# Optimization experiments

Hardware: AMD Instinct MI355X
Metric: run time of the kernel (lower is better)

Reference implementation:

```python
import jax, jax.numpy as jnp
import numpy as np

N = 100_000   # nodes
E = 640_000   # edges
H = 128       # hidden_dim
L = 4         # num_layers
C = 2         # num_classes
G = 128       # graphs in batch

def setup_inputs() -> dict:
    key = jax.random.key(0)
    ks = jax.random.split(key, 8)
    x = jax.random.randint(ks[0], (N, 1), 0, 2)
    edge_index = jax.random.randint(ks[1], (2, E), 0, N)
    batch = jnp.sort(jax.random.randint(ks[2], (N,), 0, G))
    embed = jax.random.normal(ks[3], (2, H), jnp.float32)
    Ws = jax.random.normal(ks[4], (L, H, H), jnp.float32) * (1.0 / np.sqrt(H))
    bs = jnp.zeros((L, H), jnp.float32)
    W_out = jax.random.normal(ks[5], (H, C), jnp.float32) * (1.0 / np.sqrt(H))
    b_out = jnp.zeros((C,), jnp.float32)
    return dict(x=x, edge_index=edge_index, batch=batch, embed=embed,
                Ws=Ws, bs=bs, W_out=W_out, b_out=b_out)

def reference(x, edge_index, batch, embed, Ws, bs, W_out, b_out):
    src, dst = edge_index[0], edge_index[1]
    # symmetric GCN normalization with self-loops (PyG GCNConv default)
    deg = jax.ops.segment_sum(jnp.ones(E, jnp.float32), dst, num_segments=N) + 1.0
    dinv = jax.lax.rsqrt(deg)
    enorm = (dinv[src] * dinv[dst])[:, None]   # per-edge norm
    snorm = (dinv * dinv)[:, None]             # self-loop norm

    h = embed[x[:, 0]]                          # [N, H] embedding lookup
    n_layers = Ws.shape[0]
    for l in range(n_layers):
        t = h @ Ws[l]                           # linear transform [N, H]
        agg = jax.ops.segment_sum(t[src] * enorm, dst, num_segments=N) \
              + t * snorm + bs[l]
        h = jax.nn.relu(agg) if l < n_layers - 1 else agg

    # global mean pool over graph ids
    counts = jax.ops.segment_sum(jnp.ones(N, jnp.float32), batch, num_segments=G)
    pooled = jax.ops.segment_sum(h, batch, num_segments=G) \
             / jnp.maximum(counts, 1.0)[:, None]   # [G, H]
    return pooled @ W_out + b_out                  # [G, C]
```

## Files before the change

kernel.cpp:

```cpp
#include <hip/hip_runtime.h>

typedef __attribute__((ext_vector_type(8))) short bf16x8;
typedef __attribute__((ext_vector_type(4))) float f32x4;
typedef __attribute__((ext_vector_type(2))) float f32x2;

__device__ inline unsigned short bf16_rtn(float f) {
  unsigned u = __float_as_uint(f);
  unsigned r = u + 0x7fffu + ((u >> 16) & 1u);
  return (unsigned short)(r >> 16);
}

__device__ inline void split_bf16(float f, unsigned short& hi, unsigned short& lo) {
  hi = bf16_rtn(f);
  float fh = __uint_as_float((unsigned)hi << 16);
  lo = bf16_rtn(f - fh);
}

__device__ inline float bf16_to_f(unsigned short v) {
  return __uint_as_float((unsigned)v << 16);
}

__device__ inline unsigned char f_to_fp8(float f) {
  int r = __builtin_amdgcn_cvt_pk_fp8_f32(f, f, 0, false);
  return (unsigned char)(r & 0xff);
}
__device__ inline f32x2 fp8x2_to_f(unsigned short v) {
  return __builtin_amdgcn_cvt_pk_f32_fp8((int)v, false);
}

__global__ void k_init(int* __restrict__ deg, int* __restrict__ gpz, int N, int M,
                       const float* __restrict__ Ws, const float* __restrict__ embed,
                       unsigned short* __restrict__ wphi,
                       unsigned short* __restrict__ wplo,
                       float* __restrict__ T) {
  int i = blockIdx.x * 256 + threadIdx.x;
  if (i < N) deg[i] = 0;
  if (i < M) gpz[i] = 0;
  int l = blockIdx.x;
  if (l < 3) {
    const float* W = Ws + (size_t)(l + 1) * 128 * 128;
    unsigned short* dh = wphi + (size_t)l * 16384;
    unsigned short* dl = wplo + (size_t)l * 16384;
    for (int idx = threadIdx.x; idx < 16384; idx += 256) {
      int j = idx & 7;
      int lane = (idx >> 3) & 63;
      int c = (idx >> 9) & 3;
      int ct = idx >> 11;
      int k = c * 32 + ((lane >> 4) * 8) + j;
      int n = ct * 16 + (lane & 15);
      unsigned short hi, lo;
      split_bf16(W[k * 128 + n], hi, lo);
      dh[idx] = hi;
      dl[idx] = lo;
    }
  } else if (l == 3) {
    int t = threadIdx.x;
    int r = t >> 7, c = t & 127;
    float acc = 0.f;
    for (int k = 0; k < 128; ++k)
      acc += embed[r * 128 + k] * Ws[k * 128 + c];
    T[r * 128 + c] = acc;
  }
}


__global__ void k_hist(const int* __restrict__ dst, int* __restrict__ deg,
                       int* __restrict__ posr, int E) {
  int e = blockIdx.x * 256 + threadIdx.x;
  if (e < E) posr[e] = atomicAdd(&deg[dst[e]], 1);
}

__global__ void k_scan1(const int* __restrict__ deg, int* __restrict__ rowptr,
                        int* __restrict__ bsum, float* __restrict__ dpk,
                        const int* __restrict__ x, const int* __restrict__ batch,
                        int* __restrict__ gstart, int* __restrict__ gend, int N) {
  __shared__ int s[256];
  int t = threadIdx.x;
  int i = blockIdx.x * 256 + t;
  int v = (i < N) ? deg[i] : 0;
  if (i < N) {
    float di = rsqrtf((float)v + 1.0f);
    dpk[i] = x[i] ? -di : di;
    int g = batch[i];
    if (i == 0 || batch[i - 1] != g) gstart[g] = i;
    if (i == N - 1 || batch[i + 1] != g) gend[g] = i + 1;
  }
  s[t] = v;
  __syncthreads();
  for (int off = 1; off < 256; off <<= 1) {
    int u = (t >= off) ? s[t - off] : 0;
    __syncthreads();
    s[t] += u;
    __syncthreads();
  }
  if (i < N) rowptr[i] = s[t] - v;
  if (t == 255) bsum[blockIdx.x] = s[255];
}

__global__ void k_scan2(const int* __restrict__ bsum, int* __restrict__ boff, int nb) {
  __shared__ int s[512];
  int t = threadIdx.x;
  int v = (t < nb) ? bsum[t] : 0;
  s[t] = v;
  __syncthreads();
  for (int off = 1; off < 512; off <<= 1) {
    int u = (t >= off) ? s[t - off] : 0;
    __syncthreads();
    s[t] += u;
    __syncthreads();
  }
  boff[t] = s[t] - v;
}

__global__ void k_scan3(int* __restrict__ rowptr, const int* __restrict__ boff,
                        int N, int E) {
  int i = blockIdx.x * 256 + threadIdx.x;
  if (i < N) rowptr[i] += boff[i >> 8];
  if (i == 0) rowptr[N] = E;
}

__global__ void k_scatter(const int* __restrict__ src, const int* __restrict__ dst,
                          const int* __restrict__ posr, const int* __restrict__ rowptr,
                          const float* __restrict__ dpk,
                          int2* __restrict__ epack, int E) {
  int e = blockIdx.x * 256 + threadIdx.x;
  if (e >= E) return;
  int s = src[e], d = dst[e];
  int pos = rowptr[d] + posr[e];
  epack[pos] = make_int2(s, __float_as_int(dpk[s]));
}

__device__ inline void gather_node(const unsigned char* __restrict__ tin,
                                   const int2* __restrict__ epack,
                                   int r0, int deg, int lane,
                                   float& a0, float& a1) {
  int dcap = deg < 64 ? deg : 64;
  int sl = 0;
  if (lane < dcap) sl = epack[r0 + lane].x;
  a0 = 0.f; a1 = 0.f;
  int e = 0;
  for (; e + 4 <= dcap; e += 4) {
    int s0 = __shfl(sl, e, 64),     s1 = __shfl(sl, e + 1, 64);
    int s2 = __shfl(sl, e + 2, 64), s3 = __shfl(sl, e + 3, 64);
    unsigned short p0 = *(const unsigned short*)(tin + (size_t)s0 * 128 + 2 * lane);
    unsigned short p1 = *(const unsigned short*)(tin + (size_t)s1 * 128 + 2 * lane);
    unsigned short p2 = *(const unsigned short*)(tin + (size_t)s2 * 128 + 2 * lane);
    unsigned short p3 = *(const unsigned short*)(tin + (size_t)s3 * 128 + 2 * lane);
    f32x2 v0 = fp8x2_to_f(p0), v1 = fp8x2_to_f(p1);
    f32x2 v2 = fp8x2_to_f(p2), v3 = fp8x2_to_f(p3);
    a0 += v0.x + v1.x + v2.x + v3.x;
    a1 += v0.y + v1.y + v2.y + v3.y;
  }
  for (; e < dcap; ++e) {
    int s = __shfl(sl, e, 64);
    unsigned short p = *(const unsigned short*)(tin + (size_t)s * 128 + 2 * lane);
    f32x2 v = fp8x2_to_f(p);
    a0 += v.x;
    a1 += v.y;
  }
  for (int ee = r0 + 64; ee < r0 + deg; ++ee) {
    int s = epack[ee].x;
    unsigned short p = *(const unsigned short*)(tin + (size_t)s * 128 + 2 * lane);
    f32x2 v = fp8x2_to_f(p);
    a0 += v.x;
    a1 += v.y;
  }
}

__global__ void k_agg(const unsigned char* __restrict__ tin,
                      const int* __restrict__ rowptr,
                      const int2* __restrict__ epack,
                      const float* __restrict__ dpk, const float* __restrict__ bvec,
                      unsigned short* __restrict__ h, int N) {
  int i = (blockIdx.x * blockDim.x + threadIdx.x) >> 6;
  int lane = threadIdx.x & 63;
  if (i >= N) return;
  int r0 = rowptr[i], r1 = rowptr[i + 1];
  unsigned short ps = *(const unsigned short*)(tin + (size_t)i * 128 + 2 * lane);
  float dp = dpk[i];
  float2 bv = *(const float2*)(bvec + 2 * lane);
  float a0, a1;
  gather_node(tin, epack, r0, r1 - r0, lane, a0, a1);
  f32x2 sv = fp8x2_to_f(ps);
  float di = fabsf(dp);
  a0 = fmaxf(di * (a0 + sv.x) + bv.x, 0.f);
  a1 = fmaxf(di * (a1 + sv.y) + bv.y, 0.f);
  *(unsigned*)(h + (size_t)i * 128 + 2 * lane) =
      (unsigned)bf16_rtn(a0) | ((unsigned)bf16_rtn(a1) << 16);
}

__global__ void k_agg_pool(const unsigned char* __restrict__ tin,
                           const int* __restrict__ rowptr,
                           const int2* __restrict__ epack,
                           const float* __restrict__ dpk, const float* __restrict__ bvec,
                           const int* __restrict__ batch,
                           float* __restrict__ pooled, int N) {
  __shared__ float sh[4][128];
  __shared__ int sg[4];
  int wave = threadIdx.x >> 6;
  int lane = threadIdx.x & 63;
  int i = blockIdx.x * 4 + wave;
  if (threadIdx.x < 4) sg[threadIdx.x] = -1;
  __syncthreads();
  if (i < N) {
    int r0 = rowptr[i], r1 = rowptr[i + 1];
    unsigned short ps = *(const unsigned short*)(tin + (size_t)i * 128 + 2 * lane);
    float dp = dpk[i];
    float2 bv = *(const float2*)(bvec + 2 * lane);
    float a0, a1;
    gather_node(tin, epack, r0, r1 - r0, lane, a0, a1);
    f32x2 sv = fp8x2_to_f(ps);
    float di = fabsf(dp);
    sh[wave][2 * lane]     = di * (a0 + sv.x) + bv.x;
    sh[wave][2 * lane + 1] = di * (a1 + sv.y) + bv.y;
    if (lane == 0) sg[wave] = batch[i];
  }
  __syncthreads();
  if (threadIdx.x < 128) {
    int c = threadIdx.x;
    float acc = 0.f;
    int cur = sg[0];
    #pragma unroll
    for (int w2 = 0; w2 < 4; ++w2) {
      int gw = sg[w2];
      if (gw < 0) break;
      if (gw != cur) {
        atomicAdd(&pooled[cur * 128 + c], acc);
        acc = 0.f;
        cur = gw;
      }
      acc += sh[w2][c];
    }
    atomicAdd(&pooled[cur * 128 + c], acc);
  }
}

__global__ void k_gemm(const unsigned short* __restrict__ h,
                       const unsigned short* __restrict__ wphi,
                       const unsigned short* __restrict__ wplo,
                       const float* __restrict__ dpk,
                       unsigned char* __restrict__ tout, int N) {
  int wave = threadIdx.x >> 6;
  int lane = threadIdx.x & 63;
  int r0 = (blockIdx.x * 4 + wave) * 32;
  if (r0 >= N) return;
  int q = lane >> 4;
  int m = lane & 15;
  const bf16x8* bh_base = (const bf16x8*)wphi;
  const bf16x8* bl_base = (const bf16x8*)wplo;

  f32x4 acc[2][8];
  #pragma unroll
  for (int tt = 0; tt < 2; ++tt)
    #pragma unroll
    for (int ct = 0; ct < 8; ++ct)
      acc[tt][ct] = (f32x4){0.f, 0.f, 0.f, 0.f};

  for (int c = 0; c < 4; ++c) {
    bf16x8 a0 = *(const bf16x8*)(h + (size_t)(r0 + m) * 128 + c * 32 + q * 8);
    bf16x8 a1 = *(const bf16x8*)(h + (size_t)(r0 + 16 + m) * 128 + c * 32 + q * 8);
    #pragma unroll
    for (int ct = 0; ct < 8; ++ct) {
      bf16x8 bh = bh_base[(ct * 4 + c) * 64 + lane];
      bf16x8 bl = bl_base[(ct * 4 + c) * 64 + lane];
      acc[0][ct] = __builtin_amdgcn_mfma_f32_16x16x32_bf16(a0, bh, acc[0][ct], 0, 0, 0);
      acc[0][ct] = __builtin_amdgcn_mfma_f32_16x16x32_bf16(a0, bl, acc[0][ct], 0, 0, 0);
      acc[1][ct] = __builtin_amdgcn_mfma_f32_16x16x32_bf16(a1, bh, acc[1][ct], 0, 0, 0);
      acc[1][ct] = __builtin_amdgcn_mfma_f32_16x16x32_bf16(a1, bl, acc[1][ct], 0, 0, 0);
    }
  }

  #pragma unroll
  for (int tt = 0; tt < 2; ++tt)
    #pragma unroll
    for (int ct = 0; ct < 8; ++ct)
      #pragma unroll
      for (int r = 0; r < 4; ++r) {
        int row = r0 + tt * 16 + q * 4 + r;
        if (row < N) {
          float sc = fabsf(dpk[row]);
          tout[(size_t)row * 128 + ct * 16 + m] = f_to_fp8(sc * acc[tt][ct][r]);
        }
      }
}

__device__ inline void gemm_tile8(const unsigned short* hT,
                                  const unsigned short* __restrict__ wphi,
                                  const unsigned short* __restrict__ wplo,
                                  const float* __restrict__ dpk,
                                  unsigned char* __restrict__ tout, int i0, int N) {
  int ct = threadIdx.x >> 6;
  int lane = threadIdx.x & 63;
  int q = lane >> 4;
  int m = lane & 15;
  const bf16x8* bh_base = (const bf16x8*)wphi;
  const bf16x8* bl_base = (const bf16x8*)wplo;

  f32x4 acc0 = (f32x4){0.f, 0.f, 0.f, 0.f};
  f32x4 acc1 = (f32x4){0.f, 0.f, 0.f, 0.f};

  #pragma unroll
  for (int c = 0; c < 4; ++c) {
    bf16x8 a0 = *(const bf16x8*)(hT + (m) * 136 + c * 32 + q * 8);
    bf16x8 a1 = *(const bf16x8*)(hT + (16 + m) * 136 + c * 32 + q * 8);
    bf16x8 bh = bh_base[(ct * 4 + c) * 64 + lane];
    bf16x8 bl = bl_base[(ct * 4 + c) * 64 + lane];
    acc0 = __builtin_amdgcn_mfma_f32_16x16x32_bf16(a0, bh, acc0, 0, 0, 0);
    acc0 = __builtin_amdgcn_mfma_f32_16x16x32_bf16(a0, bl, acc0, 0, 0, 0);
    acc1 = __builtin_amdgcn_mfma_f32_16x16x32_bf16(a1, bh, acc1, 0, 0, 0);
    acc1 = __builtin_amdgcn_mfma_f32_16x16x32_bf16(a1, bl, acc1, 0, 0, 0);
  }

  #pragma unroll
  for (int r = 0; r < 4; ++r) {
    int row0 = i0 + q * 4 + r;
    int row1 = row0 + 16;
    if (row0 < N) {
      float sc = fabsf(dpk[row0]);
      tout[(size_t)row0 * 128 + ct * 16 + m] = f_to_fp8(sc * acc0[r]);
    }
    if (row1 < N) {
      float sc = fabsf(dpk[row1]);
      tout[(size_t)row1 * 128 + ct * 16 + m] = f_to_fp8(sc * acc1[r]);
    }
  }
}

__global__ __launch_bounds__(512)
void k_l1_gemm(const int* __restrict__ rowptr,
               const int2* __restrict__ epack,
               const float* __restrict__ dpk, const float* __restrict__ T,
               const float* __restrict__ b0,
               const unsigned short* __restrict__ wphi,
               const unsigned short* __restrict__ wplo,
               unsigned char* __restrict__ tout, int N) {
  __shared__ unsigned short hT[32 * 136];
  int wave = threadIdx.x >> 6;
  int lane = threadIdx.x & 63;
  int i0 = blockIdx.x * 32;

  for (int j = wave * 4; j < wave * 4 + 4; ++j) {
    int i = i0 + j;
    if (i >= N) break;
    int r0 = rowptr[i], r1 = rowptr[i + 1];
    float sabs = 0.f, sneg = 0.f;
    for (int e = r0 + lane; e < r1; e += 64) {
      float wv = __int_as_float(epack[e].y);
      float aw = fabsf(wv);
      sabs += aw;
      if (wv < 0.f) sneg += aw;
    }
    for (int mm = 32; mm >= 1; mm >>= 1) {
      sabs += __shfl_xor(sabs, mm, 64);
      sneg += __shfl_xor(sneg, mm, 64);
    }
    float dp = dpk[i];
    float di = fabsf(dp);
    float sn = di * di;
    float c1 = di * sneg;
    float c0 = di * (sabs - sneg);
    if (dp < 0.f) c1 += sn; else c0 += sn;
    float v0 = fmaxf(c0 * T[2 * lane]     + c1 * T[128 + 2 * lane]     + b0[2 * lane],     0.f);
    float v1 = fmaxf(c0 * T[2 * lane + 1] + c1 * T[128 + 2 * lane + 1] + b0[2 * lane + 1], 0.f);
    *(unsigned*)&hT[j * 136 + 2 * lane] = (unsigned)bf16_rtn(v0) | ((unsigned)bf16_rtn(v1) << 16);
  }
  __syncthreads();
  gemm_tile8(hT, wphi, wplo, dpk, tout, i0, N);
}

__global__ void k_out(const float* __restrict__ pooled, const int* __restrict__ gstart,
                      const int* __restrict__ gend, const float* __restrict__ W_out,
                      const float* __restrict__ b_out, float* __restrict__ out, int G) {
  __shared__ float sp[128];
  int g = blockIdx.x;
  int j = threadIdx.x;
  float cnt = (float)(gend[g] - gstart[g]);
  sp[j] = pooled[g * 128 + j] / fmaxf(cnt, 1.f);
  __syncthreads();
  if (j < 2) {
    float o = b_out[j];
    for (int k = 0; k < 128; ++k)
      o += sp[k] * W_out[k * 2 + j];
    out[g * 2 + j] = o;
  }
}

extern "C" void kernel_launch(void* const* d_in, const int* in_sizes, int n_in,
                              void* d_out, int out_size, void* d_ws, size_t ws_size,
                              hipStream_t stream) {
  const int*   x     = (const int*)d_in[0];
  const int*   ei    = (const int*)d_in[1];
  const int*   batch = (const int*)d_in[2];
  const float* embed = (const float*)d_in[3];
  const float* Ws    = (const float*)d_in[4];
  const float* bs    = (const float*)d_in[5];
  const float* W_out = (const float*)d_in[6];
  const float* b_out = (const float*)d_in[7];
  float* out = (float*)d_out;

  int N = in_sizes[2];
  int E = in_sizes[1] / 2;
  int G = out_size / 2;

  const int* src = ei;
  const int* dst = ei + E;

  char* w = (char*)d_ws;
  auto alloc = [&](size_t bytes) {
    char* p = w;
    w += (bytes + 255) & ~(size_t)255;
    return p;
  };
  int*   deg    = (int*)  alloc((size_t)N * 4);
  float* dpk    = (float*)alloc((size_t)N * 4);
  int*   rowptr = (int*)  alloc((size_t)(N + 1) * 4);
  int*   posr   = (int*)  alloc((size_t)E * 4);
  int*   bsum   = (int*)  alloc(512 * 4);
  int*   boff   = (int*)  alloc(512 * 4);
  int*   gstart = (int*)  alloc((size_t)G * 4);
  int*   gend   = (int*)  alloc((size_t)G * 4);
  float* pooled = (float*)alloc((size_t)G * 128 * 4);
  float* T      = (float*)alloc(256 * 4);
  unsigned short* wphi = (unsigned short*)alloc((size_t)3 * 16384 * 2);
  unsigned short* wplo = (unsigned short*)alloc((size_t)3 * 16384 * 2);
  int2*  epack  = (int2*) alloc((size_t)E * 8);
  unsigned short* h = (unsigned short*)alloc((size_t)N * 128 * 2);
  unsigned char* t_a = (unsigned char*)alloc((size_t)N * 128);
  unsigned char* t_b = (unsigned char*)alloc((size_t)N * 128);

  int nbN = (N + 255) / 256;
  int nbE = (E + 255) / 256;
  int ntile = (N + 31) / 32;
  int nwb = (N + 3) / 4;
  int ngemm = (N + 127) / 128;
  int M = G * 130;

  k_init<<<nbN, 256, 0, stream>>>(deg, gstart, N, M, Ws, embed, wphi, wplo, T);
  k_hist<<<nbE, 256, 0, stream>>>(dst, deg, posr, E);
  k_scan1<<<nbN, 256, 0, stream>>>(deg, rowptr, bsum, dpk, x, batch, gstart, gend, N);
  k_scan2<<<1, 512, 0, stream>>>(bsum, boff, nbN);
  k_scan3<<<nbN, 256, 0, stream>>>(rowptr, boff, N, E);
  k_scatter<<<nbE, 256, 0, stream>>>(src, dst, posr, rowptr, dpk, epack, E);

  k_l1_gemm<<<ntile, 512, 0, stream>>>(rowptr, epack, dpk, T, bs,
                                       wphi, wplo, t_a, N);
  k_agg<<<nwb, 256, 0, stream>>>(t_a, rowptr, epack, dpk, bs + 128, h, N);
  k_gemm<<<ngemm, 256, 0, stream>>>(h, wphi + 16384, wplo + 16384, dpk, t_b, N);
  k_agg<<<nwb, 256, 0, stream>>>(t_b, rowptr, epack, dpk, bs + 256, h, N);
  k_gemm<<<ngemm, 256, 0, stream>>>(h, wphi + 32768, wplo + 32768, dpk, t_a, N);
  k_agg_pool<<<nwb, 256, 0, stream>>>(t_a, rowptr, epack, dpk, bs + 384,
                                      batch, pooled, N);
  k_out<<<G, 128, 0, stream>>>(pooled, gstart, gend, W_out, b_out, out, G);
}
```

Baseline: 334.4 us.

## Aggregate eight nodes per wave with 16-byte fp8 row loads and padded zero row

The aggregation kernels now give each node to 8 lanes instead of a full 64-lane wave. Each lane loads 16 fp8 values per neighbour with uint4 loads and keeps 16 float accumulators. The first 16 neighbours are gathered branch-free and fully unrolled: missing edges point to a zero row appended at index N, which k_init clears. The aim is to cut idle lanes and narrow 2-byte loads on low-degree nodes (average degree about 6.4) and to keep more loads in flight, at the cost of more registers and redundant loads of the zero row for nodes with few neighbours.

```diff
diff --git a/kernel.cpp b/kernel.cpp
--- a/kernel.cpp
+++ b/kernel.cpp
@@ -32,7 +32,9 @@
                        const float* __restrict__ Ws, const float* __restrict__ embed,
                        unsigned short* __restrict__ wphi,
                        unsigned short* __restrict__ wplo,
-                       float* __restrict__ T) {
+                       float* __restrict__ T,
+                       unsigned char* __restrict__ t_a,
+                       unsigned char* __restrict__ t_b) {
   int i = blockIdx.x * 256 + threadIdx.x;
   if (i < N) deg[i] = 0;
   if (i < M) gpz[i] = 0;
@@ -60,6 +62,10 @@
     for (int k = 0; k < 128; ++k)
       acc += embed[r * 128 + k] * Ws[k * 128 + c];
     T[r * 128 + c] = acc;
+  } else if (l == 4) {
+    int t = threadIdx.x;
+    if (t < 32)      ((unsigned*)(t_a + (size_t)N * 128))[t] = 0u;
+    else if (t < 64) ((unsigned*)(t_b + (size_t)N * 128))[t - 32] = 0u;
   }
 }
 
@@ -130,90 +136,121 @@
   epack[pos] = make_int2(s, __float_as_int(dpk[s]));
 }
 
-__device__ inline void gather_node(const unsigned char* __restrict__ tin,
-                                   const int2* __restrict__ epack,
-                                   int r0, int deg, int lane,
-                                   float& a0, float& a1) {
-  int dcap = deg < 64 ? deg : 64;
-  int sl = 0;
-  if (lane < dcap) sl = epack[r0 + lane].x;
-  a0 = 0.f; a1 = 0.f;
-  int e = 0;
-  for (; e + 4 <= dcap; e += 4) {
-    int s0 = __shfl(sl, e, 64),     s1 = __shfl(sl, e + 1, 64);
-    int s2 = __shfl(sl, e + 2, 64), s3 = __shfl(sl, e + 3, 64);
-    unsigned short p0 = *(const unsigned short*)(tin + (size_t)s0 * 128 + 2 * lane);
-    unsigned short p1 = *(const unsigned short*)(tin + (size_t)s1 * 128 + 2 * lane);
-    unsigned short p2 = *(const unsigned short*)(tin + (size_t)s2 * 128 + 2 * lane);
-    unsigned short p3 = *(const unsigned short*)(tin + (size_t)s3 * 128 + 2 * lane);
-    f32x2 v0 = fp8x2_to_f(p0), v1 = fp8x2_to_f(p1);
-    f32x2 v2 = fp8x2_to_f(p2), v3 = fp8x2_to_f(p3);
-    a0 += v0.x + v1.x + v2.x + v3.x;
-    a1 += v0.y + v1.y + v2.y + v3.y;
-  }
-  for (; e < dcap; ++e) {
-    int s = __shfl(sl, e, 64);
-    unsigned short p = *(const unsigned short*)(tin + (size_t)s * 128 + 2 * lane);
-    f32x2 v = fp8x2_to_f(p);
-    a0 += v.x;
-    a1 += v.y;
-  }
-  for (int ee = r0 + 64; ee < r0 + deg; ++ee) {
-    int s = epack[ee].x;
-    unsigned short p = *(const unsigned short*)(tin + (size_t)s * 128 + 2 * lane);
-    f32x2 v = fp8x2_to_f(p);
-    a0 += v.x;
-    a1 += v.y;
-  }
-}
-
-__global__ void k_agg(const unsigned char* __restrict__ tin,
-                      const int* __restrict__ rowptr,
-                      const int2* __restrict__ epack,
-                      const float* __restrict__ dpk, const float* __restrict__ bvec,
-                      unsigned short* __restrict__ h, int N) {
-  int i = (blockIdx.x * blockDim.x + threadIdx.x) >> 6;
+
+__device__ inline void acc16(float* a, uint4 p) {
+  f32x2 v;
+  v = __builtin_amdgcn_cvt_pk_f32_fp8((int)p.x, false); a[0]  += v.x; a[1]  += v.y;
+  v = __builtin_amdgcn_cvt_pk_f32_fp8((int)p.x, true);  a[2]  += v.x; a[3]  += v.y;
+  v = __builtin_amdgcn_cvt_pk_f32_fp8((int)p.y, false); a[4]  += v.x; a[5]  += v.y;
+  v = __builtin_amdgcn_cvt_pk_f32_fp8((int)p.y, true);  a[6]  += v.x; a[7]  += v.y;
+  v = __builtin_amdgcn_cvt_pk_f32_fp8((int)p.z, false); a[8]  += v.x; a[9]  += v.y;
+  v = __builtin_amdgcn_cvt_pk_f32_fp8((int)p.z, true);  a[10] += v.x; a[11] += v.y;
+  v = __builtin_amdgcn_cvt_pk_f32_fp8((int)p.w, false); a[12] += v.x; a[13] += v.y;
+  v = __builtin_amdgcn_cvt_pk_f32_fp8((int)p.w, true);  a[14] += v.x; a[15] += v.y;
+}
+
+__device__ inline void gather8(const unsigned char* __restrict__ tin,
+                               const int2* __restrict__ epack,
+                               int r0, int deg, int l8, int N,
+                               float* a) {
+  int dcap = deg < 16 ? deg : 16;
+  int slo = N, shi = N;
+  if (2 * l8 < dcap)     slo = epack[r0 + 2 * l8].x;
+  if (2 * l8 + 1 < dcap) shi = epack[r0 + 2 * l8 + 1].x;
+
+  uint4 p[16];
+  #pragma unroll
+  for (int k = 0; k < 8; ++k) {
+    int se = __shfl(slo, k, 8);
+    int so = __shfl(shi, k, 8);
+    p[2 * k]     = *(const uint4*)(tin + (size_t)((unsigned)se * 128u + ((unsigned)l8 << 4)));
+    p[2 * k + 1] = *(const uint4*)(tin + (size_t)((unsigned)so * 128u + ((unsigned)l8 << 4)));
+  }
+  #pragma unroll
+  for (int k = 0; k < 16; ++k) acc16(a, p[k]);
+
+  if (__builtin_expect(deg > 16, 0)) {
+    for (int e = r0 + 16; e < r0 + deg; ++e) {
+      int s = epack[e].x;
+      uint4 q = *(const uint4*)(tin + (size_t)((unsigned)s * 128u + ((unsigned)l8 << 4)));
+      acc16(a, q);
+    }
+  }
+}
+
+__global__ __launch_bounds__(256)
+void k_agg(const unsigned char* __restrict__ tin,
+           const int* __restrict__ rowptr,
+           const int2* __restrict__ epack,
+           const float* __restrict__ dpk, const float* __restrict__ bvec,
+           unsigned short* __restrict__ h, int N) {
   int lane = threadIdx.x & 63;
+  int g8 = lane >> 3, l8 = lane & 7;
+  int wid = (blockIdx.x * 256 + threadIdx.x) >> 6;
+  int i = wid * 8 + g8;
   if (i >= N) return;
   int r0 = rowptr[i], r1 = rowptr[i + 1];
-  unsigned short ps = *(const unsigned short*)(tin + (size_t)i * 128 + 2 * lane);
+  uint4 ps = *(const uint4*)(tin + (size_t)i * 128 + (l8 << 4));
   float dp = dpk[i];
-  float2 bv = *(const float2*)(bvec + 2 * lane);
-  float a0, a1;
-  gather_node(tin, epack, r0, r1 - r0, lane, a0, a1);
-  f32x2 sv = fp8x2_to_f(ps);
+
+  float a[16];
+  #pragma unroll
+  for (int k = 0; k < 16; ++k) a[k] = 0.f;
+  gather8(tin, epack, r0, r1 - r0, l8, N, a);
+  acc16(a, ps);
+
   float di = fabsf(dp);
-  a0 = fmaxf(di * (a0 + sv.x) + bv.x, 0.f);
-  a1 = fmaxf(di * (a1 + sv.y) + bv.y, 0.f);
-  *(unsigned*)(h + (size_t)i * 128 + 2 * lane) =
-      (unsigned)bf16_rtn(a0) | ((unsigned)bf16_rtn(a1) << 16);
-}
-
-__global__ void k_agg_pool(const unsigned char* __restrict__ tin,
-                           const int* __restrict__ rowptr,
-                           const int2* __restrict__ epack,
-                           const float* __restrict__ dpk, const float* __restrict__ bvec,
-                           const int* __restrict__ batch,
-                           float* __restrict__ pooled, int N) {
-  __shared__ float sh[4][128];
-  __shared__ int sg[4];
-  int wave = threadIdx.x >> 6;
+  const float4* bp = (const float4*)(bvec + 16 * l8);
+  float4 b0 = bp[0], b1 = bp[1], b2 = bp[2], b3 = bp[3];
+  float bb[16] = {b0.x, b0.y, b0.z, b0.w, b1.x, b1.y, b1.z, b1.w,
+                  b2.x, b2.y, b2.z, b2.w, b3.x, b3.y, b3.z, b3.w};
+  unsigned u[8];
+  #pragma unroll
+  for (int k = 0; k < 8; ++k) {
+    float v0 = fmaxf(di * a[2 * k]     + bb[2 * k],     0.f);
+    float v1 = fmaxf(di * a[2 * k + 1] + bb[2 * k + 1], 0.f);
+    u[k] = (unsigned)bf16_rtn(v0) | ((unsigned)bf16_rtn(v1) << 16);
+  }
+  uint4* hp = (uint4*)(h + (size_t)i * 128 + 16 * l8);
+  hp[0] = make_uint4(u[0], u[1], u[2], u[3]);
+  hp[1] = make_uint4(u[4], u[5], u[6], u[7]);
+}
+
+__global__ __launch_bounds__(256)
+void k_agg_pool(const unsigned char* __restrict__ tin,
+                const int* __restrict__ rowptr,
+                const int2* __restrict__ epack,
+                const float* __restrict__ dpk, const float* __restrict__ bvec,
+                const int* __restrict__ batch,
+                float* __restrict__ pooled, int N) {
+  __shared__ float sh[32][128];
+  __shared__ int sg[32];
   int lane = threadIdx.x & 63;
-  int i = blockIdx.x * 4 + wave;
-  if (threadIdx.x < 4) sg[threadIdx.x] = -1;
+  int g8 = lane >> 3, l8 = lane & 7;
+  int nloc = (threadIdx.x >> 6) * 8 + g8;
+  int i = blockIdx.x * 32 + nloc;
+  if (threadIdx.x < 32) sg[threadIdx.x] = -1;
   __syncthreads();
   if (i < N) {
     int r0 = rowptr[i], r1 = rowptr[i + 1];
-    unsigned short ps = *(const unsigned short*)(tin + (size_t)i * 128 + 2 * lane);
+    uint4 ps = *(const uint4*)(tin + (size_t)i * 128 + (l8 << 4));
     float dp = dpk[i];
-    float2 bv = *(const float2*)(bvec + 2 * lane);
-    float a0, a1;
-    gather_node(tin, epack, r0, r1 - r0, lane, a0, a1);
-    f32x2 sv = fp8x2_to_f(ps);
+
+    float a[16];
+    #pragma unroll
+    for (int k = 0; k < 16; ++k) a[k] = 0.f;
+    gather8(tin, epack, r0, r1 - r0, l8, N, a);
+    acc16(a, ps);
+
     float di = fabsf(dp);
-    sh[wave][2 * lane]     = di * (a0 + sv.x) + bv.x;
-    sh[wave][2 * lane + 1] = di * (a1 + sv.y) + bv.y;
-    if (lane == 0) sg[wave] = batch[i];
+    const float4* bp = (const float4*)(bvec + 16 * l8);
+    float4 b0 = bp[0], b1 = bp[1], b2 = bp[2], b3 = bp[3];
+    float bb[16] = {b0.x, b0.y, b0.z, b0.w, b1.x, b1.y, b1.z, b1.w,
+                    b2.x, b2.y, b2.z, b2.w, b3.x, b3.y, b3.z, b3.w};
+    #pragma unroll
+    for (int k = 0; k < 16; ++k)
+      sh[nloc][16 * l8 + k] = di * a[k] + bb[k];
+    if (l8 == 0) sg[nloc] = batch[i];
   }
   __syncthreads();
   if (threadIdx.x < 128) {
@@ -221,7 +258,7 @@
     float acc = 0.f;
     int cur = sg[0];
     #pragma unroll
-    for (int w2 = 0; w2 < 4; ++w2) {
+    for (int w2 = 0; w2 < 32; ++w2) {
       int gw = sg[w2];
       if (gw < 0) break;
       if (gw != cur) {
@@ -425,17 +462,17 @@
   unsigned short* wplo = (unsigned short*)alloc((size_t)3 * 16384 * 2);
   int2*  epack  = (int2*) alloc((size_t)E * 8);
   unsigned short* h = (unsigned short*)alloc((size_t)N * 128 * 2);
-  unsigned char* t_a = (unsigned char*)alloc((size_t)N * 128);
-  unsigned char* t_b = (unsigned char*)alloc((size_t)N * 128);
+  unsigned char* t_a = (unsigned char*)alloc((size_t)(N + 1) * 128);
+  unsigned char* t_b = (unsigned char*)alloc((size_t)(N + 1) * 128);
 
   int nbN = (N + 255) / 256;
   int nbE = (E + 255) / 256;
   int ntile = (N + 31) / 32;
-  int nwb = (N + 3) / 4;
+  int nagg = (N + 31) / 32;
   int ngemm = (N + 127) / 128;
   int M = G * 130;
 
-  k_init<<<nbN, 256, 0, stream>>>(deg, gstart, N, M, Ws, embed, wphi, wplo, T);
+  k_init<<<nbN, 256, 0, stream>>>(deg, gstart, N, M, Ws, embed, wphi, wplo, T, t_a, t_b);
   k_hist<<<nbE, 256, 0, stream>>>(dst, deg, posr, E);
   k_scan1<<<nbN, 256, 0, stream>>>(deg, rowptr, bsum, dpk, x, batch, gstart, gend, N);
   k_scan2<<<1, 512, 0, stream>>>(bsum, boff, nbN);
@@ -444,11 +481,11 @@
 
   k_l1_gemm<<<ntile, 512, 0, stream>>>(rowptr, epack, dpk, T, bs,
                                        wphi, wplo, t_a, N);
-  k_agg<<<nwb, 256, 0, stream>>>(t_a, rowptr, epack, dpk, bs + 128, h, N);
+  k_agg<<<nagg, 256, 0, stream>>>(t_a, rowptr, epack, dpk, bs + 128, h, N);
   k_gemm<<<ngemm, 256, 0, stream>>>(h, wphi + 16384, wplo + 16384, dpk, t_b, N);
-  k_agg<<<nwb, 256, 0, stream>>>(t_b, rowptr, epack, dpk, bs + 256, h, N);
+  k_agg<<<nagg, 256, 0, stream>>>(t_b, rowptr, epack, dpk, bs + 256, h, N);
   k_gemm<<<ngemm, 256, 0, stream>>>(h, wphi + 32768, wplo + 32768, dpk, t_a, N);
-  k_agg_pool<<<nwb, 256, 0, stream>>>(t_a, rowptr, epack, dpk, bs + 384,
-                                      batch, pooled, N);
+  k_agg_pool<<<nagg, 256, 0, stream>>>(t_a, rowptr, epack, dpk, bs + 384,
+                                       batch, pooled, N);
   k_out<<<G, 128, 0, stream>>>(pooled, gstart, gend, W_out, b_out, out, G);
 }
```

Measured after the change: 288.1 us. 13.8% less time.
